# Performance work log

Measured on AMD Instinct MI355X. Metric: run time of the kernel, lower is better.

Reference implementation:

```python
import jax, jax.numpy as jnp
import numpy as np

E = 23  # unique experts
K = 3   # activated experts per token


def setup_inputs() -> dict:
    key = jax.random.key(0)
    ks = jax.random.split(key, 8)
    B, S, D, H = 4, 1024, 1024, 768
    sd = 1.0 / np.sqrt(D)
    sh = 1.0 / np.sqrt(H)
    return {
        "x": jax.random.normal(ks[0], (B, S, D), jnp.float32),
        "gate_W": jax.random.normal(ks[1], (D, E), jnp.float32) * sd,
        "gate_b": jnp.zeros((E,), jnp.float32),
        "route_bias": jnp.zeros((E,), jnp.float32),  # registered buffer 'bias'
        "W1": jax.random.normal(ks[2], (E, D, H), jnp.float32) * sd,
        "b1": jnp.zeros((E, H), jnp.float32),
        "W2": jax.random.normal(ks[3], (E, H, D), jnp.float32) * sh,
        "b2": jnp.zeros((E, D), jnp.float32),
        "sW1": jax.random.normal(ks[4], (D, H), jnp.float32) * sd,
        "sb1": jnp.zeros((H,), jnp.float32),
        "sW2": jax.random.normal(ks[5], (H, D), jnp.float32) * sh,
        "sb2": jnp.zeros((D,), jnp.float32),
    }


def _gelu(x):
    return jax.nn.gelu(x, approximate=False)  # torch nn.GELU default = exact erf


def reference(x, gate_W, gate_b, route_bias, W1, b1, W2, b2, sW1, sb1, sW2, sb2):
    o_shape = x.shape
    xt = x.reshape(-1, o_shape[-1])                       # [N, D]
    N = xt.shape[0]
    gate_weights = jax.nn.sigmoid(xt @ gate_W + gate_b)   # [N, E]
    _, top_idx = jax.lax.top_k(gate_weights + route_bias, K)  # [N, K]
    top_w = jnp.take_along_axis(gate_weights, top_idx, axis=-1)
    top_w = top_w / top_w.sum(axis=-1, keepdims=True)     # [N, K]
    onehot = jax.nn.one_hot(top_idx, E, dtype=xt.dtype)   # [N, K, E]
    combine = jnp.einsum('nke,nk->ne', onehot, top_w)     # [N, E] routed weights
    counts = onehot.sum(axis=(0, 1))                      # tokens per expert
    # dense-equivalent grouped expert MLPs (same math as gather/split/concat)
    h = _gelu(jnp.einsum('nd,edh->enh', xt, W1) + b1[:, None, :])   # [E, N, H]
    y = jnp.einsum('enh,ehd->end', h, W2) + b2[:, None, :]          # [E, N, D]
    routed = jnp.einsum('end,ne->nd', y, combine)
    shared = _gelu(xt @ sW1 + sb1) @ sW2 + sb2
    out = shared + routed
    # aux load-balance loss
    gw_norm = gate_weights / gate_weights.sum(axis=-1, keepdims=True)
    P = gw_norm.mean(axis=0)
    Fvec = (E * counts) / (K * N)
    aux_loss = (P * Fvec).sum()
    return out.reshape(o_shape), aux_loss
```

## Files before the change

kernel.cpp:

```cpp
#include <hip/hip_runtime.h>
#include <hip/hip_bf16.h>
#include <stdint.h>

#define N_TOK 4096
#define DDIM  1024
#define HDIM  768
#define NEXP  23
#define TOPK  3
#define MAXTILE 152
#define SLOTS   19456

typedef float floatx4 __attribute__((ext_vector_type(4)));
typedef short short8  __attribute__((ext_vector_type(8)));

__device__ __forceinline__ short f2bf(float f) {
    __hip_bfloat16 h = __float2bfloat16(f);
    return *reinterpret_cast<short*>(&h);
}
__device__ __forceinline__ float bf2f(short s) {
    unsigned u = ((unsigned)(unsigned short)s) << 16;
    return __uint_as_float(u);
}
__device__ __forceinline__ float gelu_erf(float v) {
    return 0.5f * v * (1.0f + erff(v * 0.70710678118654752f));
}
__device__ __forceinline__ void gl_lds16(const short* g, short* l) {
    __builtin_amdgcn_global_load_lds(
        (const __attribute__((address_space(1))) void*)g,
        (__attribute__((address_space(3))) void*)l, 16, 0, 0);
}

#define PREP_GATE   1024
#define PREP_XCVT   N_TOK
#define PREP_BIAS   168
#define PREP_TCVT   2304
#define PREP_GRID   (PREP_GATE + PREP_XCVT + PREP_BIAS + PREP_TCVT)

__global__ __launch_bounds__(256) void prep_kernel(
    const float* __restrict__ x, const float* __restrict__ gate_W,
    const float* __restrict__ gate_b, const float* __restrict__ route_bias,
    int* __restrict__ top_idx, float* __restrict__ top_w,
    float* __restrict__ psum_part, short* __restrict__ xb,
    const float* __restrict__ b1, const float* __restrict__ sb1,
    const float* __restrict__ b2, const float* __restrict__ sb2,
    float* __restrict__ bias1_all, float* __restrict__ bias2_all,
    const float* __restrict__ W1, const float* __restrict__ sW1, short* __restrict__ W1T,
    const float* __restrict__ W2, const float* __restrict__ sW2, short* __restrict__ W2T)
{
    __shared__ float ps[4][NEXP];
    const int b = blockIdx.x;
    if (b >= PREP_GATE) {
        const int bb = b - PREP_GATE;
        if (bb < PREP_XCVT) {
            size_t i = (size_t)bb * 256 + threadIdx.x;
            float4 v = ((const float4*)x)[i];
            short4 o;
            o.x = f2bf(v.x); o.y = f2bf(v.y); o.z = f2bf(v.z); o.w = f2bf(v.w);
            ((short4*)xb)[i] = o;
        } else if (bb < PREP_XCVT + PREP_BIAS) {
            int i = (bb - PREP_XCVT) * 256 + threadIdx.x;
            if (i < 24 * HDIM) {
                bias1_all[i] = (i < NEXP * HDIM) ? b1[i] : sb1[i - NEXP * HDIM];
            } else {
                int j = i - 24 * HDIM;
                if (j < 24 * DDIM)
                    bias2_all[j] = (j < NEXP * DDIM) ? b2[j] : sb2[j - NEXP * DDIM];
            }
        } else {
            int idx = bb - (PREP_XCVT + PREP_BIAS);
            const float* s; short* d; int R, C, rt, ct;
            if (idx < 24 * 48) {
                const int wz = idx / 48, rem = idx % 48;
                R = DDIM; C = HDIM;
                rt = (rem / 6) * 128; ct = (rem % 6) * 128;
                s = (wz < NEXP) ? W1 + (size_t)wz * DDIM * HDIM : sW1;
                d = W1T + (size_t)wz * DDIM * HDIM;
            } else {
                idx -= 24 * 48;
                const int wz = idx / 48, rem = idx % 48;
                R = HDIM; C = DDIM;
                rt = (rem / 8) * 128; ct = (rem % 8) * 128;
                s = (wz < NEXP) ? W2 + (size_t)wz * HDIM * DDIM : sW2;
                d = W2T + (size_t)wz * HDIM * DDIM;
            }
            const int t = threadIdx.x;
            const int u = t & 15, q = t >> 4;
            const int r0 = rt + 8 * u, c0 = ct + 8 * q;
            float4 f[8][2];
#pragma unroll
            for (int i = 0; i < 8; i++) {
                f[i][0] = *(const float4*)&s[(size_t)(r0 + i) * C + c0];
                f[i][1] = *(const float4*)&s[(size_t)(r0 + i) * C + c0 + 4];
            }
#pragma unroll
            for (int j = 0; j < 8; j++) {
                const int hh = j >> 2, jj = j & 3;
                short8 col;
#pragma unroll
                for (int i = 0; i < 8; i++) {
                    float v = (jj == 0) ? f[i][hh].x :
                              (jj == 1) ? f[i][hh].y :
                              (jj == 2) ? f[i][hh].z : f[i][hh].w;
                    col[i] = f2bf(v);
                }
                *(short8*)&d[(size_t)(c0 + j) * R + r0] = col;
            }
        }
        return;
    }
    const int wave = threadIdx.x >> 6, lane = threadIdx.x & 63;
    const int n = b * 4 + wave;

    float acc[NEXP];
#pragma unroll
    for (int e = 0; e < NEXP; e++) acc[e] = 0.f;

    const float* xr = x + (size_t)n * DDIM;
#pragma unroll 4
    for (int c = 0; c < DDIM / 64; c++) {
        const int d = c * 64 + lane;
        const float xd = xr[d];
        const float* wrow = gate_W + (size_t)d * NEXP;
#pragma unroll
        for (int e = 0; e < NEXP; e++) acc[e] = fmaf(xd, wrow[e], acc[e]);
    }
    for (int off = 32; off > 0; off >>= 1) {
#pragma unroll
        for (int e = 0; e < NEXP; e++) acc[e] += __shfl_xor(acc[e], off, 64);
    }

    float p[NEXP], s = 0.f;
#pragma unroll
    for (int e = 0; e < NEXP; e++) {
        p[e] = 1.f / (1.f + expf(-(acc[e] + gate_b[e])));
        s += p[e];
    }
    const float inv = 1.f / s;

    if (lane == 0) {
#pragma unroll
        for (int e = 0; e < NEXP; e++) ps[wave][e] = p[e] * inv;
        int idx[TOPK]; float w[TOPK]; bool used[NEXP] = {};
        for (int k = 0; k < TOPK; k++) {
            float best = -1e30f; int bi = 0;
            for (int e = 0; e < NEXP; e++) {
                if (!used[e]) {
                    float sc = p[e] + route_bias[e];
                    if (sc > best) { best = sc; bi = e; }
                }
            }
            used[bi] = true; idx[k] = bi; w[k] = p[bi];
        }
        float wsum = w[0] + w[1] + w[2];
        for (int k = 0; k < TOPK; k++) {
            top_idx[n * TOPK + k] = idx[k];
            top_w[n * TOPK + k]   = w[k] / wsum;
        }
    }
    __syncthreads();
    if (threadIdx.x < NEXP) {
        int e = threadIdx.x;
        psum_part[(size_t)b * NEXP + e] =
            ps[0][e] + ps[1][e] + ps[2][e] + ps[3][e];
    }
}

__global__ __launch_bounds__(256) void plan_kernel(
    const int* __restrict__ top_idx, const float* __restrict__ psum_part,
    int* __restrict__ tile_e, int* __restrict__ tok_of_slot,
    int* __restrict__ slot_of_tok, float* __restrict__ out_aux)
{
    __shared__ int   cnt[NEXP];
    __shared__ float psum[NEXP];
    __shared__ int   tbase[NEXP + 1];
    __shared__ int   lcur[NEXP];
    const int t = threadIdx.x;
    if (t < NEXP) { cnt[t] = 0; psum[t] = 0.f; lcur[t] = 0; }
    __syncthreads();

    for (int i = t; i < N_TOK * TOPK; i += 256)
        atomicAdd(&cnt[top_idx[i]], 1);

    float loc[NEXP];
#pragma unroll
    for (int e = 0; e < NEXP; e++) loc[e] = 0.f;
    for (int b = t; b < N_TOK / 4; b += 256) {
        const float* row = psum_part + (size_t)b * NEXP;
#pragma unroll
        for (int e = 0; e < NEXP; e++) loc[e] += row[e];
    }
#pragma unroll
    for (int e = 0; e < NEXP; e++) atomicAdd(&psum[e], loc[e]);
    __syncthreads();

    if (t == 0) {
        int tb = 0; float aux = 0.f;
        for (int e = 0; e < NEXP; e++) {
            tbase[e] = tb;
            float P = psum[e] / (float)N_TOK;
            float F = (float)NEXP * (float)cnt[e] / ((float)TOPK * (float)N_TOK);
            aux += P * F;
            tb += (cnt[e] + 127) >> 7;
        }
        tbase[NEXP] = tb;
        *out_aux = aux;
    }
    __syncthreads();
    const int tr = tbase[NEXP];
    const int P  = tr << 7;
    for (int i = t; i < MAXTILE; i += 256) {
        int v = -1;
        if (i < tr) {
            for (int e = 0; e < NEXP; e++)
                if (i >= tbase[e] && i < tbase[e + 1]) v = e;
        } else if (i < tr + N_TOK / 128) v = NEXP;
        tile_e[i] = v;
    }
    for (int i = t; i < N_TOK * TOPK; i += 256) {
        const int e = top_idx[i];
        const int pos = atomicAdd(&lcur[e], 1);
        const int slot = (tbase[e] << 7) + pos;
        const int n = i / 3, k = i - n * 3;
        tok_of_slot[slot] = n;
        slot_of_tok[n * 4 + k] = slot;
    }
    for (int n = t; n < N_TOK; n += 256) {
        tok_of_slot[P + n] = n;
        slot_of_tok[n * 4 + 3] = P + n;
    }
}

template <bool FFN1>
__global__ __launch_bounds__(256) void gemm_kernel(
    const short* __restrict__ Abase, const int* __restrict__ tok_of_slot,
    const int* __restrict__ tile_e, const short* __restrict__ Wall,
    const float* __restrict__ bias_all, short* __restrict__ outb)
{
    constexpr int KD = FFN1 ? DDIM : HDIM;
    constexpr int NC = FFN1 ? HDIM : DDIM;
    constexpr int KI = KD / 32;
    constexpr int GX = NC / 128;
    constexpr int NWG = GX * MAXTILE;
    constexpr int Q = NWG / 8, RM = NWG % 8;

    int bid = blockIdx.y * GX + blockIdx.x;
    {
        const int xcd = bid & 7, off = bid >> 3;
        bid = (xcd < RM) ? (xcd * (Q + 1) + off)
                         : (RM * (Q + 1) + (xcd - RM) * Q + off);
    }
    const int tile = bid / GX;
    const int e = tile_e[tile];
    if (e < 0) return;
    const int slot0 = tile * 128;
    const int n0 = (bid - tile * GX) * 128;

    __shared__ short smem[3 * 4096 * 2];
    short* const As = smem;
    short* const Bs = smem + 3 * 4096;

    const int t = threadIdx.x;
    const int w = t >> 6, l = t & 63;
    const int quad = l >> 4, l16 = l & 15;
    const int wr = w >> 1, wc = w & 1;

    const int ra0 = w * 32 + (l >> 2);
    const int ra1 = ra0 + 16;
    const int ko  = (l & 3) << 3;

    const short *ap0, *ap1;
    if constexpr (FFN1) {
        int t0 = tok_of_slot[slot0 + ra0];
        int t1 = tok_of_slot[slot0 + ra1];
        t0 = ((unsigned)t0 < (unsigned)N_TOK) ? t0 : 0;
        t1 = ((unsigned)t1 < (unsigned)N_TOK) ? t1 : 0;
        ap0 = Abase + (size_t)t0 * KD + ko;
        ap1 = Abase + (size_t)t1 * KD + ko;
    } else {
        ap0 = Abase + (size_t)(slot0 + ra0) * KD + ko;
        ap1 = Abase + (size_t)(slot0 + ra1) * KD + ko;
    }
    const short* bbase = Wall + (size_t)e * NC * KD + (size_t)n0 * KD;
    const short* bp0 = bbase + (size_t)ra0 * KD + ko;
    const short* bp1 = bbase + (size_t)ra1 * KD + ko;

    const int ldo0 = (w * 32) * 32;
    const int ldo1 = (w * 32 + 16) * 32;

    floatx4 acc[4][4] = {};

#pragma unroll
    for (int p = 0; p < 3; p++) {
        gl_lds16(ap0, As + p * 4096 + ldo0); gl_lds16(ap1, As + p * 4096 + ldo1);
        gl_lds16(bp0, Bs + p * 4096 + ldo0); gl_lds16(bp1, Bs + p * 4096 + ldo1);
        ap0 += 32; ap1 += 32; bp0 += 32; bp1 += 32;
    }

#pragma unroll
    for (int k = 0; k < KI; k++) {
        if (k < KI - 2)       asm volatile("s_waitcnt vmcnt(8)" ::: "memory");
        else if (k == KI - 2) asm volatile("s_waitcnt vmcnt(4)" ::: "memory");
        else                  asm volatile("s_waitcnt vmcnt(0)" ::: "memory");
        asm volatile("s_barrier" ::: "memory");

        const int s = k % 3;
        short8 af[4], bf[4];
#pragma unroll
        for (int i = 0; i < 4; i++)
            af[i] = *(const short8*)(As + s * 4096 + (wr * 64 + i * 16 + l16) * 32 + quad * 8);
#pragma unroll
        for (int j = 0; j < 4; j++)
            bf[j] = *(const short8*)(Bs + s * 4096 + (wc * 64 + j * 16 + l16) * 32 + quad * 8);
#pragma unroll
        for (int i = 0; i < 4; i++)
#pragma unroll
            for (int j = 0; j < 4; j++)
                acc[i][j] = __builtin_amdgcn_mfma_f32_16x16x32_bf16(af[i], bf[j], acc[i][j], 0, 0, 0);

        asm volatile("s_waitcnt lgkmcnt(0)" ::: "memory");
        asm volatile("s_barrier" ::: "memory");
        if (k + 3 < KI) {
            gl_lds16(ap0, As + s * 4096 + ldo0); gl_lds16(ap1, As + s * 4096 + ldo1);
            gl_lds16(bp0, Bs + s * 4096 + ldo0); gl_lds16(bp1, Bs + s * 4096 + ldo1);
            ap0 += 32; ap1 += 32; bp0 += 32; bp1 += 32;
        }
    }

    short* const OT = smem;
    const int bias_off = e * NC + n0;
#pragma unroll
    for (int j = 0; j < 4; j++) {
        const int colL = wc * 64 + j * 16 + l16;
        const float bv = bias_all[bias_off + colL];
        const int cg = colL >> 3, wi = colL & 7;
#pragma unroll
        for (int i = 0; i < 4; i++)
#pragma unroll
            for (int r = 0; r < 4; r++) {
                const int rowL = wr * 64 + i * 16 + quad * 4 + r;
                float v = acc[i][j][r] + bv;
                if constexpr (FFN1) v = gelu_erf(v);
                OT[rowL * 128 + (((cg ^ ((rowL >> 2) & 3)) << 3) | wi)] = f2bf(v);
            }
    }
    __syncthreads();
#pragma unroll
    for (int p = 0; p < 8; p++) {
        const int rowL = p * 16 + (t >> 4);
        const int g = t & 15;
        const short8 v = *(const short8*)(OT + rowL * 128 + ((g ^ ((rowL >> 2) & 3)) << 3));
        *(short8*)&outb[(size_t)(slot0 + rowL) * NC + n0 + g * 8] = v;
    }
}

__global__ __launch_bounds__(256) void combine_kernel(
    const short* __restrict__ ybuf, const int* __restrict__ slot_of_tok,
    const float* __restrict__ top_w, float* __restrict__ out)
{
    const int n = blockIdx.x;
    const int c = threadIdx.x;
    const int s0 = slot_of_tok[n * 4 + 0];
    const int s1 = slot_of_tok[n * 4 + 1];
    const int s2 = slot_of_tok[n * 4 + 2];
    const int ss = slot_of_tok[n * 4 + 3];
    const float w0 = top_w[n * 3 + 0];
    const float w1 = top_w[n * 3 + 1];
    const float w2 = top_w[n * 3 + 2];

    short4 y0 = ((const short4*)(ybuf + (size_t)s0 * DDIM))[c];
    short4 y1 = ((const short4*)(ybuf + (size_t)s1 * DDIM))[c];
    short4 y2 = ((const short4*)(ybuf + (size_t)s2 * DDIM))[c];
    short4 ys = ((const short4*)(ybuf + (size_t)ss * DDIM))[c];

    float4 o;
    o.x = bf2f(ys.x) + w0 * bf2f(y0.x) + w1 * bf2f(y1.x) + w2 * bf2f(y2.x);
    o.y = bf2f(ys.y) + w0 * bf2f(y0.y) + w1 * bf2f(y1.y) + w2 * bf2f(y2.y);
    o.z = bf2f(ys.z) + w0 * bf2f(y0.z) + w1 * bf2f(y1.z) + w2 * bf2f(y2.z);
    o.w = bf2f(ys.w) + w0 * bf2f(y0.w) + w1 * bf2f(y1.w) + w2 * bf2f(y2.w);
    ((float4*)(out + (size_t)n * DDIM))[c] = o;
}

extern "C" void kernel_launch(void* const* d_in, const int* in_sizes, int n_in,
                              void* d_out, int out_size, void* d_ws, size_t ws_size,
                              hipStream_t stream)
{
    const float* x          = (const float*)d_in[0];
    const float* gate_W     = (const float*)d_in[1];
    const float* gate_b     = (const float*)d_in[2];
    const float* route_bias = (const float*)d_in[3];
    const float* W1         = (const float*)d_in[4];
    const float* b1         = (const float*)d_in[5];
    const float* W2         = (const float*)d_in[6];
    const float* b2         = (const float*)d_in[7];
    const float* sW1        = (const float*)d_in[8];
    const float* sb1        = (const float*)d_in[9];
    const float* sW2        = (const float*)d_in[10];
    const float* sb2        = (const float*)d_in[11];
    float* out = (float*)d_out;

    uint8_t* ws = (uint8_t*)d_ws;
    int*   top_idx   = (int*)(ws);
    float* top_w     = (float*)(ws + 49152);
    int*   tile_e    = (int*)(ws + 98688);
    float* psum_part = (float*)(ws + 99328);
    int*   tok_slot  = (int*)(ws + 193536);
    int*   slot_tok  = (int*)(ws + 271360);
    float* bias1_all = (float*)(ws + 336896);
    float* bias2_all = (float*)(ws + 410624);
    short* xb        = (short*)(ws + 512000);
    short* W1T       = (short*)(ws + 8902656);
    short* W2T       = (short*)(ws + 46651392);
    short* hbuf      = (short*)(ws + 84400128);
    short* ybuf      = (short*)(ws + 512000);

    prep_kernel<<<PREP_GRID, 256, 0, stream>>>(
        x, gate_W, gate_b, route_bias, top_idx, top_w, psum_part,
        xb, b1, sb1, b2, sb2, bias1_all, bias2_all,
        W1, sW1, W1T, W2, sW2, W2T);
    plan_kernel<<<1, 256, 0, stream>>>(top_idx, psum_part, tile_e,
                                       tok_slot, slot_tok,
                                       out + (size_t)N_TOK * DDIM);

    gemm_kernel<true><<<dim3(HDIM / 128, MAXTILE), 256, 0, stream>>>(
        xb, tok_slot, tile_e, W1T, bias1_all, hbuf);
    gemm_kernel<false><<<dim3(DDIM / 128, MAXTILE), 256, 0, stream>>>(
        hbuf, tok_slot, tile_e, W2T, bias2_all, ybuf);
    combine_kernel<<<N_TOK, 256, 0, stream>>>(ybuf, slot_tok, top_w, out);
}
```

Before: 410.9 us.

## Split gating into its own kernel and overlap planning with weight conversion

```diff
diff --git a/kernel.cpp b/kernel.cpp
--- a/kernel.cpp
+++ b/kernel.cpp
@@ -9,6 +9,7 @@
 #define TOPK  3
 #define MAXTILE 152
 #define SLOTS   19456
+#define GATE_BLKS 256
 
 typedef float floatx4 __attribute__((ext_vector_type(4)));
 typedef short short8  __attribute__((ext_vector_type(8)));
@@ -30,142 +31,107 @@
         (__attribute__((address_space(3))) void*)l, 16, 0, 0);
 }
 
-#define PREP_GATE   1024
-#define PREP_XCVT   N_TOK
-#define PREP_BIAS   168
-#define PREP_TCVT   2304
-#define PREP_GRID   (PREP_GATE + PREP_XCVT + PREP_BIAS + PREP_TCVT)
-
-__global__ __launch_bounds__(256) void prep_kernel(
+__global__ __launch_bounds__(256) void gate_kernel(
     const float* __restrict__ x, const float* __restrict__ gate_W,
     const float* __restrict__ gate_b, const float* __restrict__ route_bias,
     int* __restrict__ top_idx, float* __restrict__ top_w,
-    float* __restrict__ psum_part, short* __restrict__ xb,
+    float* __restrict__ psum_part)
+{
+    __shared__ float gw[512 * NEXP];
+    __shared__ float ps[4][NEXP];
+    const int t = threadIdx.x;
+    const int wave = t >> 6, lane = t & 63;
+    const int n0 = blockIdx.x * 16 + wave * 4;
+
+    float acc[4][NEXP];
+#pragma unroll
+    for (int k = 0; k < 4; k++)
+#pragma unroll
+        for (int e = 0; e < NEXP; e++) acc[k][e] = 0.f;
+
+    for (int ph = 0; ph < 2; ph++) {
+        if (ph) __syncthreads();
+        {
+            const float2* src = (const float2*)gate_W + ph * (512 * NEXP / 2);
+            float2* dst = (float2*)gw;
+            for (int i = t; i < 512 * NEXP / 2; i += 256) dst[i] = src[i];
+        }
+        __syncthreads();
+#pragma unroll
+        for (int c = 0; c < 8; c++) {
+            const int d = ph * 512 + c * 64 + lane;
+            float xd[4];
+#pragma unroll
+            for (int k = 0; k < 4; k++) xd[k] = x[(size_t)(n0 + k) * DDIM + d];
+            const float* wrow = gw + (c * 64 + lane) * NEXP;
+#pragma unroll
+            for (int e = 0; e < NEXP; e++) {
+                const float wv = wrow[e];
+#pragma unroll
+                for (int k = 0; k < 4; k++) acc[k][e] = fmaf(xd[k], wv, acc[k][e]);
+            }
+        }
+    }
+    for (int off = 32; off > 0; off >>= 1)
+#pragma unroll
+        for (int k = 0; k < 4; k++)
+#pragma unroll
+            for (int e = 0; e < NEXP; e++)
+                acc[k][e] += __shfl_xor(acc[k][e], off, 64);
+
+    if (lane == 0) {
+        float pw[NEXP];
+#pragma unroll
+        for (int e = 0; e < NEXP; e++) pw[e] = 0.f;
+        for (int k = 0; k < 4; k++) {
+            const int n = n0 + k;
+            float p[NEXP], s = 0.f;
+#pragma unroll
+            for (int e = 0; e < NEXP; e++) {
+                p[e] = 1.f / (1.f + expf(-(acc[k][e] + gate_b[e])));
+                s += p[e];
+            }
+            const float inv = 1.f / s;
+#pragma unroll
+            for (int e = 0; e < NEXP; e++) pw[e] += p[e] * inv;
+            int idx[TOPK]; float w[TOPK]; bool used[NEXP] = {};
+            for (int kk = 0; kk < TOPK; kk++) {
+                float best = -1e30f; int bi = 0;
+                for (int e = 0; e < NEXP; e++) {
+                    if (!used[e]) {
+                        float sc = p[e] + route_bias[e];
+                        if (sc > best) { best = sc; bi = e; }
+                    }
+                }
+                used[bi] = true; idx[kk] = bi; w[kk] = p[bi];
+            }
+            float wsum = w[0] + w[1] + w[2];
+            for (int kk = 0; kk < TOPK; kk++) {
+                top_idx[n * TOPK + kk] = idx[kk];
+                top_w[n * TOPK + kk]   = w[kk] / wsum;
+            }
+        }
+#pragma unroll
+        for (int e = 0; e < NEXP; e++) ps[wave][e] = pw[e];
+    }
+    __syncthreads();
+    if (t < NEXP)
+        psum_part[t * GATE_BLKS + blockIdx.x] =
+            ps[0][t] + ps[1][t] + ps[2][t] + ps[3][t];
+}
+
+#define P2_TCVT 2304
+#define P2_XCVT N_TOK
+#define P2_BIAS 168
+#define P2_GRID (1 + P2_TCVT + P2_XCVT + P2_BIAS)
+
+__global__ __launch_bounds__(256, 2) void prep2_kernel(
+    const float* __restrict__ x, short* __restrict__ xb,
     const float* __restrict__ b1, const float* __restrict__ sb1,
     const float* __restrict__ b2, const float* __restrict__ sb2,
     float* __restrict__ bias1_all, float* __restrict__ bias2_all,
     const float* __restrict__ W1, const float* __restrict__ sW1, short* __restrict__ W1T,
-    const float* __restrict__ W2, const float* __restrict__ sW2, short* __restrict__ W2T)
-{
-    __shared__ float ps[4][NEXP];
-    const int b = blockIdx.x;
-    if (b >= PREP_GATE) {
-        const int bb = b - PREP_GATE;
-        if (bb < PREP_XCVT) {
-            size_t i = (size_t)bb * 256 + threadIdx.x;
-            float4 v = ((const float4*)x)[i];
-            short4 o;
-            o.x = f2bf(v.x); o.y = f2bf(v.y); o.z = f2bf(v.z); o.w = f2bf(v.w);
-            ((short4*)xb)[i] = o;
-        } else if (bb < PREP_XCVT + PREP_BIAS) {
-            int i = (bb - PREP_XCVT) * 256 + threadIdx.x;
-            if (i < 24 * HDIM) {
-                bias1_all[i] = (i < NEXP * HDIM) ? b1[i] : sb1[i - NEXP * HDIM];
-            } else {
-                int j = i - 24 * HDIM;
-                if (j < 24 * DDIM)
-                    bias2_all[j] = (j < NEXP * DDIM) ? b2[j] : sb2[j - NEXP * DDIM];
-            }
-        } else {
-            int idx = bb - (PREP_XCVT + PREP_BIAS);
-            const float* s; short* d; int R, C, rt, ct;
-            if (idx < 24 * 48) {
-                const int wz = idx / 48, rem = idx % 48;
-                R = DDIM; C = HDIM;
-                rt = (rem / 6) * 128; ct = (rem % 6) * 128;
-                s = (wz < NEXP) ? W1 + (size_t)wz * DDIM * HDIM : sW1;
-                d = W1T + (size_t)wz * DDIM * HDIM;
-            } else {
-                idx -= 24 * 48;
-                const int wz = idx / 48, rem = idx % 48;
-                R = HDIM; C = DDIM;
-                rt = (rem / 8) * 128; ct = (rem % 8) * 128;
-                s = (wz < NEXP) ? W2 + (size_t)wz * HDIM * DDIM : sW2;
-                d = W2T + (size_t)wz * HDIM * DDIM;
-            }
-            const int t = threadIdx.x;
-            const int u = t & 15, q = t >> 4;
-            const int r0 = rt + 8 * u, c0 = ct + 8 * q;
-            float4 f[8][2];
-#pragma unroll
-            for (int i = 0; i < 8; i++) {
-                f[i][0] = *(const float4*)&s[(size_t)(r0 + i) * C + c0];
-                f[i][1] = *(const float4*)&s[(size_t)(r0 + i) * C + c0 + 4];
-            }
-#pragma unroll
-            for (int j = 0; j < 8; j++) {
-                const int hh = j >> 2, jj = j & 3;
-                short8 col;
-#pragma unroll
-                for (int i = 0; i < 8; i++) {
-                    float v = (jj == 0) ? f[i][hh].x :
-                              (jj == 1) ? f[i][hh].y :
-                              (jj == 2) ? f[i][hh].z : f[i][hh].w;
-                    col[i] = f2bf(v);
-                }
-                *(short8*)&d[(size_t)(c0 + j) * R + r0] = col;
-            }
-        }
-        return;
-    }
-    const int wave = threadIdx.x >> 6, lane = threadIdx.x & 63;
-    const int n = b * 4 + wave;
-
-    float acc[NEXP];
-#pragma unroll
-    for (int e = 0; e < NEXP; e++) acc[e] = 0.f;
-
-    const float* xr = x + (size_t)n * DDIM;
-#pragma unroll 4
-    for (int c = 0; c < DDIM / 64; c++) {
-        const int d = c * 64 + lane;
-        const float xd = xr[d];
-        const float* wrow = gate_W + (size_t)d * NEXP;
-#pragma unroll
-        for (int e = 0; e < NEXP; e++) acc[e] = fmaf(xd, wrow[e], acc[e]);
-    }
-    for (int off = 32; off > 0; off >>= 1) {
-#pragma unroll
-        for (int e = 0; e < NEXP; e++) acc[e] += __shfl_xor(acc[e], off, 64);
-    }
-
-    float p[NEXP], s = 0.f;
-#pragma unroll
-    for (int e = 0; e < NEXP; e++) {
-        p[e] = 1.f / (1.f + expf(-(acc[e] + gate_b[e])));
-        s += p[e];
-    }
-    const float inv = 1.f / s;
-
-    if (lane == 0) {
-#pragma unroll
-        for (int e = 0; e < NEXP; e++) ps[wave][e] = p[e] * inv;
-        int idx[TOPK]; float w[TOPK]; bool used[NEXP] = {};
-        for (int k = 0; k < TOPK; k++) {
-            float best = -1e30f; int bi = 0;
-            for (int e = 0; e < NEXP; e++) {
-                if (!used[e]) {
-                    float sc = p[e] + route_bias[e];
-                    if (sc > best) { best = sc; bi = e; }
-                }
-            }
-            used[bi] = true; idx[k] = bi; w[k] = p[bi];
-        }
-        float wsum = w[0] + w[1] + w[2];
-        for (int k = 0; k < TOPK; k++) {
-            top_idx[n * TOPK + k] = idx[k];
-            top_w[n * TOPK + k]   = w[k] / wsum;
-        }
-    }
-    __syncthreads();
-    if (threadIdx.x < NEXP) {
-        int e = threadIdx.x;
-        psum_part[(size_t)b * NEXP + e] =
-            ps[0][e] + ps[1][e] + ps[2][e] + ps[3][e];
-    }
-}
-
-__global__ __launch_bounds__(256) void plan_kernel(
+    const float* __restrict__ W2, const float* __restrict__ sW2, short* __restrict__ W2T,
     const int* __restrict__ top_idx, const float* __restrict__ psum_part,
     int* __restrict__ tile_e, int* __restrict__ tok_of_slot,
     int* __restrict__ slot_of_tok, float* __restrict__ out_aux)
@@ -174,59 +140,118 @@
     __shared__ float psum[NEXP];
     __shared__ int   tbase[NEXP + 1];
     __shared__ int   lcur[NEXP];
+    const int b = blockIdx.x;
     const int t = threadIdx.x;
-    if (t < NEXP) { cnt[t] = 0; psum[t] = 0.f; lcur[t] = 0; }
-    __syncthreads();
-
-    for (int i = t; i < N_TOK * TOPK; i += 256)
-        atomicAdd(&cnt[top_idx[i]], 1);
-
-    float loc[NEXP];
-#pragma unroll
-    for (int e = 0; e < NEXP; e++) loc[e] = 0.f;
-    for (int b = t; b < N_TOK / 4; b += 256) {
-        const float* row = psum_part + (size_t)b * NEXP;
-#pragma unroll
-        for (int e = 0; e < NEXP; e++) loc[e] += row[e];
-    }
-#pragma unroll
-    for (int e = 0; e < NEXP; e++) atomicAdd(&psum[e], loc[e]);
-    __syncthreads();
-
-    if (t == 0) {
-        int tb = 0; float aux = 0.f;
+
+    if (b == 0) {
+        if (t < NEXP) { cnt[t] = 0; psum[t] = 0.f; lcur[t] = 0; }
+        __syncthreads();
+
+        const int4* ti4 = (const int4*)top_idx;
+        for (int i = t; i < N_TOK * TOPK / 4; i += 256) {
+            int4 v = ti4[i];
+            atomicAdd(&cnt[v.x], 1); atomicAdd(&cnt[v.y], 1);
+            atomicAdd(&cnt[v.z], 1); atomicAdd(&cnt[v.w], 1);
+        }
+#pragma unroll
         for (int e = 0; e < NEXP; e++) {
-            tbase[e] = tb;
-            float P = psum[e] / (float)N_TOK;
-            float F = (float)NEXP * (float)cnt[e] / ((float)TOPK * (float)N_TOK);
-            aux += P * F;
-            tb += (cnt[e] + 127) >> 7;
-        }
-        tbase[NEXP] = tb;
-        *out_aux = aux;
-    }
-    __syncthreads();
-    const int tr = tbase[NEXP];
-    const int P  = tr << 7;
-    for (int i = t; i < MAXTILE; i += 256) {
-        int v = -1;
-        if (i < tr) {
-            for (int e = 0; e < NEXP; e++)
-                if (i >= tbase[e] && i < tbase[e + 1]) v = e;
-        } else if (i < tr + N_TOK / 128) v = NEXP;
-        tile_e[i] = v;
-    }
-    for (int i = t; i < N_TOK * TOPK; i += 256) {
-        const int e = top_idx[i];
-        const int pos = atomicAdd(&lcur[e], 1);
-        const int slot = (tbase[e] << 7) + pos;
-        const int n = i / 3, k = i - n * 3;
-        tok_of_slot[slot] = n;
-        slot_of_tok[n * 4 + k] = slot;
-    }
-    for (int n = t; n < N_TOK; n += 256) {
-        tok_of_slot[P + n] = n;
-        slot_of_tok[n * 4 + 3] = P + n;
+            float v = psum_part[e * GATE_BLKS + t];
+            for (int off = 32; off > 0; off >>= 1) v += __shfl_xor(v, off, 64);
+            if ((t & 63) == 0) atomicAdd(&psum[e], v);
+        }
+        __syncthreads();
+
+        if (t == 0) {
+            int tb = 0; float aux = 0.f;
+            for (int e = 0; e < NEXP; e++) {
+                tbase[e] = tb;
+                float P = psum[e] / (float)N_TOK;
+                float F = (float)NEXP * (float)cnt[e] / ((float)TOPK * (float)N_TOK);
+                aux += P * F;
+                tb += (cnt[e] + 127) >> 7;
+            }
+            tbase[NEXP] = tb;
+            *out_aux = aux;
+        }
+        __syncthreads();
+        const int tr = tbase[NEXP];
+        const int P  = tr << 7;
+        for (int i = t; i < MAXTILE; i += 256) {
+            int v = -1;
+            if (i < tr) {
+                for (int e = 0; e < NEXP; e++)
+                    if (i >= tbase[e] && i < tbase[e + 1]) v = e;
+            } else if (i < tr + N_TOK / 128) v = NEXP;
+            tile_e[i] = v;
+        }
+        for (int i = t; i < N_TOK * TOPK; i += 256) {
+            const int e = top_idx[i];
+            const int pos = atomicAdd(&lcur[e], 1);
+            const int slot = (tbase[e] << 7) + pos;
+            const int n = i / 3, k = i - n * 3;
+            tok_of_slot[slot] = n;
+            slot_of_tok[n * 4 + k] = slot;
+        }
+        for (int n = t; n < N_TOK; n += 256) {
+            tok_of_slot[P + n] = n;
+            slot_of_tok[n * 4 + 3] = P + n;
+        }
+        return;
+    }
+    const int bb = b - 1;
+    if (bb < P2_TCVT) {
+        int idx = bb;
+        const float* s; short* d; int R, C, rt, ct;
+        if (idx < 24 * 48) {
+            const int wz = idx / 48, rem = idx % 48;
+            R = DDIM; C = HDIM;
+            rt = (rem / 6) * 128; ct = (rem % 6) * 128;
+            s = (wz < NEXP) ? W1 + (size_t)wz * DDIM * HDIM : sW1;
+            d = W1T + (size_t)wz * DDIM * HDIM;
+        } else {
+            idx -= 24 * 48;
+            const int wz = idx / 48, rem = idx % 48;
+            R = HDIM; C = DDIM;
+            rt = (rem / 8) * 128; ct = (rem % 8) * 128;
+            s = (wz < NEXP) ? W2 + (size_t)wz * HDIM * DDIM : sW2;
+            d = W2T + (size_t)wz * HDIM * DDIM;
+        }
+        const int u = t & 15, q = t >> 4;
+        const int r0 = rt + 8 * u, c0 = ct + 8 * q;
+        float4 f[8][2];
+#pragma unroll
+        for (int i = 0; i < 8; i++) {
+            f[i][0] = *(const float4*)&s[(size_t)(r0 + i) * C + c0];
+            f[i][1] = *(const float4*)&s[(size_t)(r0 + i) * C + c0 + 4];
+        }
+#pragma unroll
+        for (int j = 0; j < 8; j++) {
+            const int hh = j >> 2, jj = j & 3;
+            short8 col;
+#pragma unroll
+            for (int i = 0; i < 8; i++) {
+                float v = (jj == 0) ? f[i][hh].x :
+                          (jj == 1) ? f[i][hh].y :
+                          (jj == 2) ? f[i][hh].z : f[i][hh].w;
+                col[i] = f2bf(v);
+            }
+            *(short8*)&d[(size_t)(c0 + j) * R + r0] = col;
+        }
+    } else if (bb < P2_TCVT + P2_XCVT) {
+        size_t i = (size_t)(bb - P2_TCVT) * 256 + t;
+        float4 v = ((const float4*)x)[i];
+        short4 o;
+        o.x = f2bf(v.x); o.y = f2bf(v.y); o.z = f2bf(v.z); o.w = f2bf(v.w);
+        ((short4*)xb)[i] = o;
+    } else {
+        int i = (bb - P2_TCVT - P2_XCVT) * 256 + t;
+        if (i < 24 * HDIM) {
+            bias1_all[i] = (i < NEXP * HDIM) ? b1[i] : sb1[i - NEXP * HDIM];
+        } else {
+            int j = i - 24 * HDIM;
+            if (j < 24 * DDIM)
+                bias2_all[j] = (j < NEXP * DDIM) ? b2[j] : sb2[j - NEXP * DDIM];
+        }
     }
 }
 
@@ -413,13 +438,13 @@
     short* hbuf      = (short*)(ws + 84400128);
     short* ybuf      = (short*)(ws + 512000);
 
-    prep_kernel<<<PREP_GRID, 256, 0, stream>>>(
-        x, gate_W, gate_b, route_bias, top_idx, top_w, psum_part,
-        xb, b1, sb1, b2, sb2, bias1_all, bias2_all,
-        W1, sW1, W1T, W2, sW2, W2T);
-    plan_kernel<<<1, 256, 0, stream>>>(top_idx, psum_part, tile_e,
-                                       tok_slot, slot_tok,
-                                       out + (size_t)N_TOK * DDIM);
+    gate_kernel<<<GATE_BLKS, 256, 0, stream>>>(
+        x, gate_W, gate_b, route_bias, top_idx, top_w, psum_part);
+    prep2_kernel<<<P2_GRID, 256, 0, stream>>>(
+        x, xb, b1, sb1, b2, sb2, bias1_all, bias2_all,
+        W1, sW1, W1T, W2, sW2, W2T,
+        top_idx, psum_part, tile_e, tok_slot, slot_tok,
+        out + (size_t)N_TOK * DDIM);
 
     gemm_kernel<true><<<dim3(HDIM / 128, MAXTILE), 256, 0, stream>>>(
         xb, tok_slot, tile_e, W1T, bias1_all, hbuf);
```

New measurement: 477.9 us. +16.3%, slower.
